# Performance work log

Measured on AMD Instinct MI355X. Metric: run time of the kernel, lower is better.

The kernel has to match this reference:

```python
import jax, jax.numpy as jnp
import numpy as np
from jax.scipy.special import logsumexp

LOG2PI = float(np.log(2.0 * np.pi))
N_GRID = 25  # dim == 2 -> N = 25
NEG = -1e9


def _cond_logprob(cand, hist_loc, hist_t, t, beta, sigma):
    # cand [B,M,d], hist_loc [B,H,d], hist_t [B,H], t [B]
    d = cand.shape[-1]
    logw = -beta * (t[:, None] - hist_t)                       # [B,H]
    logw = logw - logsumexp(logw, axis=1, keepdims=True)
    diff = cand[:, :, None, :] - hist_loc[:, None, :, :]       # [B,M,H,d]
    sq = jnp.sum(diff * diff, axis=-1)                         # [B,M,H]
    logN = -0.5 * sq / (sigma * sigma) - d * jnp.log(sigma) - 0.5 * d * LOG2PI
    return logsumexp(logw[:, None, :] + logN, axis=-1)         # [B,M]


def _gmm_call(times, locs, beta, sigma):
    # causal GMM loglik: event k explained by mixture over events j<k
    B, L, d = locs.shape
    dt = times[:, :, None] - times[:, None, :]                 # [B,L,L]
    mask = jnp.tril(jnp.ones((L, L), dtype=bool), -1)          # j < k
    raw = jnp.where(mask, -beta * dt, NEG)
    logw = raw - logsumexp(raw, axis=-1, keepdims=True)
    diff = locs[:, :, None, :] - locs[:, None, :, :]           # [B,L,L,d]
    sq = jnp.sum(diff * diff, axis=-1)
    logN = -0.5 * sq / (sigma * sigma) - d * jnp.log(sigma) - 0.5 * d * LOG2PI
    logp = logsumexp(jnp.where(mask, logw + logN, NEG), axis=-1)  # [B,L]
    logp0 = -0.5 * jnp.sum(locs[:, 0] ** 2, axis=-1) - 0.5 * d * LOG2PI
    return logp0 + jnp.sum(logp[:, 1:], axis=-1)               # [B]


def setup_inputs() -> dict:
    key = jax.random.key(0)
    ks = jax.random.split(key, 6)
    B, H, PLTS, D = 64, 384, 16, 2
    input_time = jnp.sort(jax.random.uniform(ks[0], (B, H), dtype=jnp.float32), axis=1)
    curr_time = 1.0 + jnp.sort(jax.random.uniform(ks[1], (B, PLTS), dtype=jnp.float32), axis=1)
    history_data = jax.random.normal(ks[2], (B, H, D), dtype=jnp.float32)
    expected_data = jax.random.normal(ks[3], (B, PLTS, D), dtype=jnp.float32)
    aux_state_in = jax.random.normal(ks[4], (B, H, 1), dtype=jnp.float32)
    aux_state_out = jax.random.normal(ks[5], (B, PLTS, 1), dtype=jnp.float32)
    beta = jnp.ones((1,), dtype=jnp.float32)
    log_sigma = jnp.zeros((1,), dtype=jnp.float32)
    return {"curr_time": curr_time, "input_time": input_time,
            "history_data": history_data, "expected_data": expected_data,
            "aux_state_in": aux_state_in, "aux_state_out": aux_state_out,
            "beta": beta, "log_sigma": log_sigma}


def reference(curr_time, input_time, history_data, expected_data,
              aux_state_in, aux_state_out, beta, log_sigma):
    sigma = jnp.exp(log_sigma)
    B, plts, d = expected_data.shape
    hist = history_data
    times = input_time
    preds = []
    for i in range(plts):
        expected_loc = expected_data[:, i, :]                  # [B,d]
        nd = jnp.concatenate([hist, expected_loc[:, None, :]], axis=1)  # [B,H+1,d]
        # faithful to source: bounds from event rows 0 and 1 (scalar min/max)
        minx, maxx = jnp.min(nd[:, 0]), jnp.max(nd[:, 0])
        miny, maxy = jnp.min(nd[:, 1]), jnp.max(nd[:, 1])
        xlim = jnp.linspace(minx, maxx, N_GRID)
        ylim = jnp.linspace(miny, maxy, N_GRID)
        X1, X2 = jnp.meshgrid(xlim, ylim)
        arr = jnp.stack([X1.reshape(-1), X2.reshape(-1)], axis=1)  # [N*N,2]
        cand = jnp.broadcast_to(arr[None], (B, N_GRID * N_GRID, 2))
        ll = _cond_logprob(cand, hist, times, curr_time[:, i], beta, sigma)  # [B,N*N]
        arg = jnp.argmin(ll, axis=-1)                          # [B]
        predicted = jnp.take_along_axis(cand, arg[:, None, None], axis=1)[:, 0, :]  # [B,2]
        preds.append(predicted)
        hist = jnp.concatenate([hist, predicted[:, None, :]], axis=1)
        times = jnp.concatenate([times, curr_time[:, i:i + 1]], axis=1)
    spatial_loglik = _gmm_call(times, hist, beta, sigma)       # [B]
    predicted_out = jnp.stack(preds, axis=0)                   # [plts,B,2]
    return spatial_loglik, predicted_out
```

## Files before the change

### kernel.cpp

```cpp
#include <hip/hip_runtime.h>
#include <hip/hip_bf16.h>
#include <math.h>

#define BB    64
#define HH    384
#define PLTS  16
#define LMAX  (HH + PLTS)
#define NG    25
#define NC    (NG * NG)
#define BLOCK 1024
#define NWAVES (BLOCK / 64)
#define FSTR  388
#define KHALF 192
#define NUNIT (2 * NC)

#if defined(__has_builtin) && __has_builtin(__builtin_amdgcn_exp2f)
static __device__ __forceinline__ float fast_exp2(float x) { return __builtin_amdgcn_exp2f(x); }
#else
static __device__ __forceinline__ float fast_exp2(float x) { return exp2f(x); }
#endif
#if defined(__has_builtin) && __has_builtin(__builtin_amdgcn_logf)
static __device__ __forceinline__ float fast_log2(float x) { return __builtin_amdgcn_logf(x); }
#else
static __device__ __forceinline__ float fast_log2(float x) { return log2f(x); }
#endif

__global__ __launch_bounds__(BLOCK)
void spatio_kernel(const float* __restrict__ ct,
                   const float* __restrict__ it,
                   const float* __restrict__ hd,
                   const float* __restrict__ beta_p,
                   const float* __restrict__ lsig_p,
                   float* __restrict__ out)
{
    __shared__ __align__(16) float FxT[NG][FSTR];
    __shared__ __align__(16) float FyT[NG][FSTR];
    __shared__ __align__(16) float u_s [LMAX];
    __shared__ __align__(16) float px_s[LMAX];
    __shared__ __align__(16) float py_s[LMAX];
    __shared__ float  w2s[LMAX];
    __shared__ float2 hxy[LMAX];
    __shared__ float  P[NUNIT];
    __shared__ float  Pg[BLOCK];
    __shared__ float  rowt[16];
    __shared__ float  pre[LMAX];
    __shared__ float  wsum[NWAVES];
    __shared__ float  rv[NWAVES];
    __shared__ float  sb[4];

    const int b    = blockIdx.x;
    const int tid  = threadIdx.x;
    const int lane = tid & 63;
    const int wave = tid >> 6;

    const float LOG2E  = 1.4426950408889634f;
    const float LN2    = 0.69314718055994531f;
    const float LOG2PI = 1.8378770664093453f;
    const float INF    = __builtin_inff();

    const float beta  = beta_p[0];
    const float lsig  = lsig_p[0];
    const float sigma = fast_exp2(lsig * LOG2E);
    const float cc    = -0.5f / (sigma * sigma);
    const float c2    = cc * LOG2E;
    const float bl    = beta * LOG2E;
    const float Sc    = -2.0f * lsig - LOG2PI;

    for (int j = tid; j < HH; j += BLOCK) {
        float t = it[b * HH + j];
        float x = hd[(b * HH + j) * 2 + 0];
        float y = hd[(b * HH + j) * 2 + 1];
        float w = bl * t;
        w2s[j]  = w;
        hxy[j]  = make_float2(x, y);
        u_s[j]  = fmaf(c2, x * x + y * y, w);
        px_s[j] = -2.0f * c2 * x;
        py_s[j] = -2.0f * c2 * y;
    }

    float wn_r[16];
    if (wave == 0) {
        const float4* ct4 = (const float4*)(ct + b * PLTS);
        float4 c0 = ct4[0], c1 = ct4[1], c2v = ct4[2], c3 = ct4[3];
        wn_r[0]=bl*c0.x;  wn_r[1]=bl*c0.y;  wn_r[2]=bl*c0.z;  wn_r[3]=bl*c0.w;
        wn_r[4]=bl*c1.x;  wn_r[5]=bl*c1.y;  wn_r[6]=bl*c1.z;  wn_r[7]=bl*c1.w;
        wn_r[8]=bl*c2v.x; wn_r[9]=bl*c2v.y; wn_r[10]=bl*c2v.z;wn_r[11]=bl*c2v.w;
        wn_r[12]=bl*c3.x; wn_r[13]=bl*c3.y; wn_r[14]=bl*c3.z; wn_r[15]=bl*c3.w;
    } else {
        #pragma unroll
        for (int k = 0; k < 16; ++k) wn_r[k] = 0.0f;
    }

    if (tid < 64) {
        const float* p = hd + tid * (HH * 2);
        float p0x = p[0], p0y = p[1], p1x = p[2], p1y = p[3];
        float xmn = fminf(p0x, p0y), xmx = fmaxf(p0x, p0y);
        float ymn = fminf(p1x, p1y), ymx = fmaxf(p1x, p1y);
        for (int o = 32; o > 0; o >>= 1) {
            xmn = fminf(xmn, __shfl_down(xmn, o, 64));
            xmx = fmaxf(xmx, __shfl_down(xmx, o, 64));
            ymn = fminf(ymn, __shfl_down(ymn, o, 64));
            ymx = fmaxf(ymx, __shfl_down(ymx, o, 64));
        }
        if (tid == 0) { sb[0] = xmn; sb[1] = xmx; sb[2] = ymn; sb[3] = ymx; }
    }
    __syncthreads();

    const float minx = sb[0], maxx = sb[1], miny = sb[2], maxy = sb[3];
    const float stepx = (maxx - minx) * (1.0f / 24.0f);
    const float stepy = (maxy - miny) * (1.0f / 24.0f);

    for (int idx = tid; idx < NG * HH; idx += BLOCK) {
        int row = idx / HH;
        int j   = idx - row * HH;
        float2 h = hxy[j];
        float cxr = fmaf((float)row, stepx, minx);
        float cyr = fmaf((float)row, stepy, miny);
        float dx = cxr - h.x;
        float dy = cyr - h.y;
        FxT[row][j] = fast_exp2(fmaf(c2 * dx, dx, w2s[j]));
        FyT[row][j] = fast_exp2(c2 * dy * dy);
    }
    __syncthreads();

    #pragma unroll
    for (int rep = 0; rep < 2; ++rep) {
        int u = tid + rep * BLOCK;
        if (u < NUNIT) {
            int h    = (u >= NC) ? 1 : 0;
            int c    = u - h * NC;
            int ky   = c / NG;
            int kx   = c - NG * ky;
            const float4* fx4 = (const float4*)&FxT[kx][0];
            const float4* fy4 = (const float4*)&FyT[ky][0];
            int g0 = h * (KHALF / 4);
            float s0 = 0.f, s1 = 0.f, s2 = 0.f, s3 = 0.f;
            #pragma unroll 8
            for (int g = g0; g < g0 + KHALF / 4; ++g) {
                float4 a = fx4[g], bv = fy4[g];
                s0 = fmaf(a.x, bv.x, s0);
                s1 = fmaf(a.y, bv.y, s1);
                s2 = fmaf(a.z, bv.z, s2);
                s3 = fmaf(a.w, bv.w, s3);
            }
            P[u] = (s0 + s1) + (s2 + s3);
        }
    }
    __syncthreads();

    if (wave == 0) {
        float Sv[10], cxk[10], cyk[10];
        const int cbase = lane * 10;
        #pragma unroll
        for (int k = 0; k < 10; ++k) {
            int c = cbase + k;
            if (c < NC) {
                Sv[k] = P[c] + P[c + NC];
                int ky = (int)((c + 0.5f) * 0.04f);
                int kx = c - 25 * ky;
                cxk[k] = fmaf((float)kx, stepx, minx);
                cyk[k] = fmaf((float)ky, stepy, miny);
            } else {
                Sv[k] = INF; cxk[k] = 0.0f; cyk[k] = 0.0f;
            }
        }
        #pragma unroll
        for (int i = 0; i < PLTS; ++i) {
            float v = Sv[0]; int ik = 0;
            #pragma unroll
            for (int k = 1; k < 10; ++k)
                if (Sv[k] < v) { v = Sv[k]; ik = k; }
            int idx = cbase + ik;
            #pragma unroll
            for (int o = 1; o < 64; o <<= 1) {
                float ov = __shfl_xor(v, o, 64);
                int   oi = __shfl_xor(idx, o, 64);
                if (ov < v || (ov == v && oi < idx)) { v = ov; idx = oi; }
            }
            int   ky = (int)((idx + 0.5f) * 0.04f);
            int   kx = idx - 25 * ky;
            float px = fmaf((float)kx, stepx, minx);
            float py = fmaf((float)ky, stepy, miny);
            float wn = wn_r[i];
            if (lane == 0) {
                const int L = HH + i;
                w2s[L]  = wn;
                hxy[L]  = make_float2(px, py);
                u_s[L]  = fmaf(c2, px * px + py * py, wn);
                px_s[L] = -2.0f * c2 * px;
                py_s[L] = -2.0f * c2 * py;
                out[BB + (i * BB + b) * 2 + 0] = px;
                out[BB + (i * BB + b) * 2 + 1] = py;
            }
            #pragma unroll
            for (int k = 0; k < 10; ++k) {
                float dx = px - cxk[k], dy = py - cyk[k];
                Sv[k] += fast_exp2(fmaf(c2, fmaf(dx, dx, dy * dy), wn));
            }
        }
    } else {
        const int t2 = tid - 64;
        int row = 0, c = 0;
        if (t2 < 100)      { row = t2 + 1; c = 0; }
        else if (t2 < 300) { int u = t2 - 100; row = 101 + (u >> 1); c = u & 1; }
        else if (t2 < 600) { int u = t2 - 300; int q = u / 3; row = 201 + q; c = u - 3 * q; }
        else if (t2 < 932) { int u = t2 - 600; row = 301 + (u >> 2); c = u & 3; }
        float part = 0.0f;
        if (row > 0) {
            int j0 = c * 100;
            int j1 = min(row, j0 + 100);
            float2 hi = hxy[row];
            float xi = hi.x, yi = hi.y;
            float Ai = c2 * fmaf(xi, xi, yi * yi);
            float a0 = 0.f, a1 = 0.f;
            int j = j0;
            for (; j + 1 < j1; j += 2) {
                a0 += fast_exp2(fmaf(px_s[j],     xi, fmaf(py_s[j],     yi, u_s[j]     + Ai)));
                a1 += fast_exp2(fmaf(px_s[j + 1], xi, fmaf(py_s[j + 1], yi, u_s[j + 1] + Ai)));
            }
            if (j < j1)
                a0 += fast_exp2(fmaf(px_s[j], xi, fmaf(py_s[j], yi, u_s[j] + Ai)));
            part = a0 + a1;
        }
        Pg[tid] = part;
    }
    __syncthreads();

    {
        const int row = HH + wave;
        int j0 = lane * 7;
        int j1 = min(row, j0 + 7);
        float2 hi = hxy[row];
        float xi = hi.x, yi = hi.y;
        float Ai = c2 * fmaf(xi, xi, yi * yi);
        float part = 0.0f;
        for (int j = j0; j < j1; ++j)
            part += fast_exp2(fmaf(px_s[j], xi, fmaf(py_s[j], yi, u_s[j] + Ai)));
        for (int o = 32; o > 0; o >>= 1) part += __shfl_down(part, o, 64);
        if (lane == 0) rowt[wave] = part;
    }

    float x = (tid < LMAX) ? fast_exp2(w2s[tid]) : 0.0f;
    for (int o = 1; o < 64; o <<= 1) {
        float y = __shfl_up(x, o, 64);
        if (lane >= o) x += y;
    }
    if (lane == 63) wsum[wave] = x;
    __syncthreads();
    float off = 0.0f;
    for (int w = 0; w < wave; ++w) off += wsum[w];
    if (tid < LMAX) pre[tid] = x + off;
    __syncthreads();

    float acc = 0.0f;
    if (tid >= 1 && tid < LMAX) {
        const int row = tid;
        float tot;
        if (row <= 100)      { tot = Pg[64 + row - 1]; }
        else if (row <= 200) { int base = 64 + 100 + (row - 101) * 2;
                               tot = Pg[base] + Pg[base + 1]; }
        else if (row <= 300) { int base = 64 + 300 + (row - 201) * 3;
                               tot = Pg[base] + Pg[base + 1] + Pg[base + 2]; }
        else if (row <= 383) { int base = 64 + 600 + (row - 301) * 4;
                               tot = (Pg[base] + Pg[base + 1]) + (Pg[base + 2] + Pg[base + 3]); }
        else                 { tot = rowt[row - HH]; }
        acc = Sc + LN2 * (fast_log2(tot) - fast_log2(pre[row - 1]));
    }
    for (int o = 32; o > 0; o >>= 1) acc += __shfl_down(acc, o, 64);
    if (lane == 0) rv[wave] = acc;
    __syncthreads();
    if (tid == 0) {
        float tot = 0.0f;
        for (int w = 0; w < NWAVES; ++w) tot += rv[w];
        float2 h0 = hxy[0];
        tot += -0.5f * (h0.x * h0.x + h0.y * h0.y) - LOG2PI;
        out[b] = tot;
    }
}

extern "C" void kernel_launch(void* const* d_in, const int* in_sizes, int n_in,
                              void* d_out, int out_size, void* d_ws, size_t ws_size,
                              hipStream_t stream) {
    const float* ct   = (const float*)d_in[0];
    const float* it   = (const float*)d_in[1];
    const float* hd   = (const float*)d_in[2];
    const float* beta = (const float*)d_in[6];
    const float* lsig = (const float*)d_in[7];
    float* out = (float*)d_out;

    hipLaunchKernelGGL(spatio_kernel, dim3(BB), dim3(BLOCK), 0, stream,
                       ct, it, hd, beta, lsig, out);
}
```

Measured before the change: 89.31 us.

## Register-block grid GEMM over 5 x-rows, DPP argmin, vectorize causal exp sums

The separable grid score product is restructured so each thread computes five candidate columns over a 48-wide K chunk. Each Fy load is reused five times, and the work is split into 8 chunks across 1000 threads; the partials are reduced with float4 reads. The per-step argmin now uses a DPP min reduction followed by ballot and readlane, replacing the xor-shuffle of value/index pairs. The causal GMM row sums read u/px/py as float4 with four accumulators. The aim is to cut LDS traffic and shuffle latency in the serial prediction loop, at the cost of more register pressure and a different floating-point summation order.

```diff
diff --git a/kernel.cpp b/kernel.cpp
--- a/kernel.cpp
+++ b/kernel.cpp
@@ -11,8 +11,9 @@
 #define BLOCK 1024
 #define NWAVES (BLOCK / 64)
 #define FSTR  388
-#define KHALF 192
-#define NUNIT (2 * NC)
+#define NCHUNK 8
+#define KC    48
+#define GEMM_UNITS (125 * NCHUNK)
 
 #if defined(__has_builtin) && __has_builtin(__builtin_amdgcn_exp2f)
 static __device__ __forceinline__ float fast_exp2(float x) { return __builtin_amdgcn_exp2f(x); }
@@ -24,6 +25,36 @@
 #else
 static __device__ __forceinline__ float fast_log2(float x) { return log2f(x); }
 #endif
+
+#if defined(__has_builtin)
+#if __has_builtin(__builtin_amdgcn_update_dpp) && __has_builtin(__builtin_amdgcn_readlane)
+#define HAS_DPP 1
+#endif
+#endif
+
+static __device__ __forceinline__ float wave_min_all(float v) {
+#ifdef HAS_DPP
+    float r = v;
+    #define DPP_STEP(ctrl) { int ri = __float_as_int(r); \
+        int si = __builtin_amdgcn_update_dpp(ri, ri, (ctrl), 0xf, 0xf, false); \
+        r = fminf(r, __int_as_float(si)); }
+    DPP_STEP(0x111) DPP_STEP(0x112) DPP_STEP(0x114) DPP_STEP(0x118)
+    DPP_STEP(0x142) DPP_STEP(0x143)
+    #undef DPP_STEP
+    return __int_as_float(__builtin_amdgcn_readlane(__float_as_int(r), 63));
+#else
+    for (int o = 1; o < 64; o <<= 1) v = fminf(v, __shfl_xor(v, o, 64));
+    return v;
+#endif
+}
+
+static __device__ __forceinline__ int lane_bcast_int(int x, int src_lane) {
+#ifdef HAS_DPP
+    return __builtin_amdgcn_readlane(x, src_lane);
+#else
+    return __shfl(x, src_lane, 64);
+#endif
+}
 
 __global__ __launch_bounds__(BLOCK)
 void spatio_kernel(const float* __restrict__ ct,
@@ -40,7 +71,7 @@
     __shared__ __align__(16) float py_s[LMAX];
     __shared__ float  w2s[LMAX];
     __shared__ float2 hxy[LMAX];
-    __shared__ float  P[NUNIT];
+    __shared__ __align__(16) float P[NC * NCHUNK];
     __shared__ float  Pg[BLOCK];
     __shared__ float  rowt[16];
     __shared__ float  pre[LMAX];
@@ -123,28 +154,44 @@
     }
     __syncthreads();
 
-    #pragma unroll
-    for (int rep = 0; rep < 2; ++rep) {
-        int u = tid + rep * BLOCK;
-        if (u < NUNIT) {
-            int h    = (u >= NC) ? 1 : 0;
-            int c    = u - h * NC;
-            int ky   = c / NG;
-            int kx   = c - NG * ky;
-            const float4* fx4 = (const float4*)&FxT[kx][0];
-            const float4* fy4 = (const float4*)&FyT[ky][0];
-            int g0 = h * (KHALF / 4);
-            float s0 = 0.f, s1 = 0.f, s2 = 0.f, s3 = 0.f;
-            #pragma unroll 8
-            for (int g = g0; g < g0 + KHALF / 4; ++g) {
-                float4 a = fx4[g], bv = fy4[g];
-                s0 = fmaf(a.x, bv.x, s0);
-                s1 = fmaf(a.y, bv.y, s1);
-                s2 = fmaf(a.z, bv.z, s2);
-                s3 = fmaf(a.w, bv.w, s3);
-            }
-            P[u] = (s0 + s1) + (s2 + s3);
-        }
+    if (tid < GEMM_UNITS) {
+        int chunk = tid / 125;
+        int r     = tid - chunk * 125;
+        int ky    = r / 5;
+        int kxg   = r - ky * 5;
+        const int g0 = chunk * (KC / 4);
+        const float4* fy4 = (const float4*)&FyT[ky][0];
+        const float4* fx0 = (const float4*)&FxT[5 * kxg + 0][0];
+        const float4* fx1 = (const float4*)&FxT[5 * kxg + 1][0];
+        const float4* fx2 = (const float4*)&FxT[5 * kxg + 2][0];
+        const float4* fx3 = (const float4*)&FxT[5 * kxg + 3][0];
+        const float4* fx4 = (const float4*)&FxT[5 * kxg + 4][0];
+        float4 A0 = {0,0,0,0}, A1 = {0,0,0,0}, A2 = {0,0,0,0}, A3 = {0,0,0,0}, A4 = {0,0,0,0};
+        #pragma unroll
+        for (int g = g0; g < g0 + KC / 4; ++g) {
+            float4 bv = fy4[g];
+            float4 x0 = fx0[g];
+            A0.x = fmaf(x0.x, bv.x, A0.x); A0.y = fmaf(x0.y, bv.y, A0.y);
+            A0.z = fmaf(x0.z, bv.z, A0.z); A0.w = fmaf(x0.w, bv.w, A0.w);
+            float4 x1 = fx1[g];
+            A1.x = fmaf(x1.x, bv.x, A1.x); A1.y = fmaf(x1.y, bv.y, A1.y);
+            A1.z = fmaf(x1.z, bv.z, A1.z); A1.w = fmaf(x1.w, bv.w, A1.w);
+            float4 x2 = fx2[g];
+            A2.x = fmaf(x2.x, bv.x, A2.x); A2.y = fmaf(x2.y, bv.y, A2.y);
+            A2.z = fmaf(x2.z, bv.z, A2.z); A2.w = fmaf(x2.w, bv.w, A2.w);
+            float4 x3 = fx3[g];
+            A3.x = fmaf(x3.x, bv.x, A3.x); A3.y = fmaf(x3.y, bv.y, A3.y);
+            A3.z = fmaf(x3.z, bv.z, A3.z); A3.w = fmaf(x3.w, bv.w, A3.w);
+            float4 x4 = fx4[g];
+            A4.x = fmaf(x4.x, bv.x, A4.x); A4.y = fmaf(x4.y, bv.y, A4.y);
+            A4.z = fmaf(x4.z, bv.z, A4.z); A4.w = fmaf(x4.w, bv.w, A4.w);
+        }
+        const int cb = 5 * kxg + 25 * ky;
+        P[(cb + 0) * NCHUNK + chunk] = (A0.x + A0.y) + (A0.z + A0.w);
+        P[(cb + 1) * NCHUNK + chunk] = (A1.x + A1.y) + (A1.z + A1.w);
+        P[(cb + 2) * NCHUNK + chunk] = (A2.x + A2.y) + (A2.z + A2.w);
+        P[(cb + 3) * NCHUNK + chunk] = (A3.x + A3.y) + (A3.z + A3.w);
+        P[(cb + 4) * NCHUNK + chunk] = (A4.x + A4.y) + (A4.z + A4.w);
     }
     __syncthreads();
 
@@ -155,7 +202,9 @@
         for (int k = 0; k < 10; ++k) {
             int c = cbase + k;
             if (c < NC) {
-                Sv[k] = P[c] + P[c + NC];
+                const float4* p4 = (const float4*)&P[c * NCHUNK];
+                float4 a = p4[0], d = p4[1];
+                Sv[k] = ((a.x + a.y) + (a.z + a.w)) + ((d.x + d.y) + (d.z + d.w));
                 int ky = (int)((c + 0.5f) * 0.04f);
                 int kx = c - 25 * ky;
                 cxk[k] = fmaf((float)kx, stepx, minx);
@@ -166,17 +215,17 @@
         }
         #pragma unroll
         for (int i = 0; i < PLTS; ++i) {
-            float v = Sv[0]; int ik = 0;
+            float vl = Sv[0];
             #pragma unroll
-            for (int k = 1; k < 10; ++k)
-                if (Sv[k] < v) { v = Sv[k]; ik = k; }
-            int idx = cbase + ik;
+            for (int k = 1; k < 10; ++k) vl = fminf(vl, Sv[k]);
+            float vmin = wave_min_all(vl);
+            unsigned long long m = __ballot(vl == vmin);
+            int win = (int)__ffsll((unsigned long long)m) - 1;
+            int kl = 9;
             #pragma unroll
-            for (int o = 1; o < 64; o <<= 1) {
-                float ov = __shfl_xor(v, o, 64);
-                int   oi = __shfl_xor(idx, o, 64);
-                if (ov < v || (ov == v && oi < idx)) { v = ov; idx = oi; }
-            }
+            for (int k = 9; k >= 0; --k) if (Sv[k] == vmin) kl = k;
+            int kwin = lane_bcast_int(kl, win);
+            int idx  = win * 10 + kwin;
             int   ky = (int)((idx + 0.5f) * 0.04f);
             int   kx = idx - 25 * ky;
             float px = fmaf((float)kx, stepx, minx);
@@ -212,15 +261,22 @@
             float2 hi = hxy[row];
             float xi = hi.x, yi = hi.y;
             float Ai = c2 * fmaf(xi, xi, yi * yi);
-            float a0 = 0.f, a1 = 0.f;
+            const float4* u4g  = (const float4*)u_s;
+            const float4* px4g = (const float4*)px_s;
+            const float4* py4g = (const float4*)py_s;
+            float a0 = 0.f, a1 = 0.f, a2 = 0.f, a3 = 0.f;
             int j = j0;
-            for (; j + 1 < j1; j += 2) {
-                a0 += fast_exp2(fmaf(px_s[j],     xi, fmaf(py_s[j],     yi, u_s[j]     + Ai)));
-                a1 += fast_exp2(fmaf(px_s[j + 1], xi, fmaf(py_s[j + 1], yi, u_s[j + 1] + Ai)));
+            for (; j + 4 <= j1; j += 4) {
+                int g = j >> 2;
+                float4 U = u4g[g], PX = px4g[g], PY = py4g[g];
+                a0 += fast_exp2(fmaf(PX.x, xi, fmaf(PY.x, yi, U.x + Ai)));
+                a1 += fast_exp2(fmaf(PX.y, xi, fmaf(PY.y, yi, U.y + Ai)));
+                a2 += fast_exp2(fmaf(PX.z, xi, fmaf(PY.z, yi, U.z + Ai)));
+                a3 += fast_exp2(fmaf(PX.w, xi, fmaf(PY.w, yi, U.w + Ai)));
             }
-            if (j < j1)
+            for (; j < j1; ++j)
                 a0 += fast_exp2(fmaf(px_s[j], xi, fmaf(py_s[j], yi, u_s[j] + Ai)));
-            part = a0 + a1;
+            part = (a0 + a1) + (a2 + a3);
         }
         Pg[tid] = part;
     }
```

After: 81.62 us. -8.6%, faster.
